# Optimization experiments

Measured on AMD Instinct MI355X. Metric: run time of the kernel, lower is better.

The kernel has to match this reference:

```python
import jax, jax.numpy as jnp
import numpy as np

D_MODEL = 256
N_HEADS = 8
N_LEVELS = 4
N_POINTS = 4
D_FFN = 1024
HW = 128
LQ = HW * HW
LIN = N_LEVELS * LQ
BATCH = 2
HEAD_DIM = D_MODEL // N_HEADS
SPATIAL = [(HW, HW)] * N_LEVELS  # static (H, W) per level
EPS = 1e-5


def _layer_norm(x, g, b):
    m = jnp.mean(x, axis=-1, keepdims=True)
    v = jnp.mean(jnp.square(x - m), axis=-1, keepdims=True)
    return (x - m) * jax.lax.rsqrt(v + EPS) * g + b


def _gather(v, idx):
    # v: (N, heads, HW, hd); idx: (N, heads, Lq, P) -> (N, heads, Lq, P, hd)
    N, Hh, Lq, P = idx.shape
    out = jnp.take_along_axis(v, idx.reshape(N, Hh, Lq * P)[..., None], axis=2)
    return out.reshape(N, Hh, Lq, P, -1)


def _ms_deform_attn_core(value, loc, attn):
    # value: (N, Lin, heads, hd); loc: (N, Lq, heads, L, P, 2) in [0,1]; attn: (N, Lq, heads, L, P)
    N, _, Hh, hd = value.shape
    Lq = loc.shape[1]
    out = jnp.zeros((N, Hh, Lq, hd), value.dtype)
    start = 0
    for l, (H, W) in enumerate(SPATIAL):
        v = value[:, start:start + H * W].transpose(0, 2, 1, 3)  # (N, heads, H*W, hd)
        start += H * W
        ll = loc[:, :, :, l].transpose(0, 2, 1, 3, 4)  # (N, heads, Lq, P, 2)
        # F.grid_sample(align_corners=False, padding_mode='zeros') on grid 2*loc-1:
        # pixel coord = loc * size - 0.5
        x = ll[..., 0] * W - 0.5
        y = ll[..., 1] * H - 0.5
        x0 = jnp.floor(x)
        y0 = jnp.floor(y)
        wx = x - x0
        wy = y - y0
        x0i = x0.astype(jnp.int32)
        y0i = y0.astype(jnp.int32)
        acc = jnp.zeros((N, Hh, Lq, N_POINTS, hd), value.dtype)
        for dy, wyc in ((0, 1.0 - wy), (1, wy)):
            for dx, wxc in ((0, 1.0 - wx), (1, wx)):
                xi = x0i + dx
                yi = y0i + dy
                valid = (xi >= 0) & (xi < W) & (yi >= 0) & (yi < H)
                idx = jnp.clip(yi, 0, H - 1) * W + jnp.clip(xi, 0, W - 1)
                g = _gather(v, idx)
                w = (wxc * wyc * valid).astype(value.dtype)
                acc = acc + g * w[..., None]
        aw = attn[:, :, :, l].transpose(0, 2, 1, 3)  # (N, heads, Lq, P)
        out = out + jnp.sum(acc * aw[..., None], axis=3)
    return out.transpose(0, 2, 1, 3).reshape(N, Lq, Hh * hd)


def _forward(cur_src, src_all, pos, reference_points, spatial_shape,
             W_off, b_off, W_attn, b_attn, W_val, b_val, W_out, b_out,
             gamma1, beta1, W1, b1, W2, b2, gamma2, beta2):
    N, Lq, d = cur_src.shape
    q = cur_src + pos[:, -1]                      # with_pos_embed(cur_src, pos[-1])
    inp = src_all + pos.reshape(N, -1, d)         # with_pos_embed(src_all, cat(pos, 1))
    value = (inp @ W_val + b_val).reshape(N, -1, N_HEADS, HEAD_DIM)
    off = (q @ W_off + b_off).reshape(N, Lq, N_HEADS, N_LEVELS, N_POINTS, 2)
    attn = (q @ W_attn + b_attn).reshape(N, Lq, N_HEADS, N_LEVELS * N_POINTS)
    attn = jax.nn.softmax(attn, axis=-1).reshape(N, Lq, N_HEADS, N_LEVELS, N_POINTS)
    # offset_normalizer = stack([W, H], -1)
    normalizer = jnp.stack([spatial_shape[..., 1], spatial_shape[..., 0]], -1).astype(cur_src.dtype)
    loc = reference_points[:, :, None, :, None, :] + off / normalizer[None, None, None, :, None, :]
    src2 = _ms_deform_attn_core(value, loc, attn) @ W_out + b_out
    src = _layer_norm(cur_src + src2, gamma1, beta1)   # dropout is identity in eval
    ffn = jax.nn.relu(src @ W1 + b1) @ W2 + b2
    return _layer_norm(src + ffn, gamma2, beta2)


def setup_inputs():
    key = jax.random.key(0)
    ks = jax.random.split(key, 16)
    s = 0.02
    f32 = jnp.float32
    return {
        "cur_src": jax.random.normal(ks[0], (BATCH, LQ, D_MODEL), f32),
        "src_all": jax.random.normal(ks[1], (BATCH, LIN, D_MODEL), f32),
        "pos": jax.random.normal(ks[2], (BATCH, N_LEVELS, LQ, D_MODEL), f32),
        "reference_points": jax.random.uniform(ks[3], (BATCH, LQ, N_LEVELS, 2), f32),
        "spatial_shape": jnp.array(SPATIAL, dtype=jnp.int32),
        "level_start_index": (jnp.arange(N_LEVELS) * LQ).astype(jnp.int32),
        "W_off": jax.random.normal(ks[4], (D_MODEL, N_HEADS * N_LEVELS * N_POINTS * 2), f32) * s,
        "b_off": jax.random.normal(ks[5], (N_HEADS * N_LEVELS * N_POINTS * 2,), f32) * 0.5,
        "W_attn": jax.random.normal(ks[6], (D_MODEL, N_HEADS * N_LEVELS * N_POINTS), f32) * s,
        "b_attn": jnp.zeros((N_HEADS * N_LEVELS * N_POINTS,), f32),
        "W_val": jax.random.normal(ks[7], (D_MODEL, D_MODEL), f32) * s,
        "b_val": jnp.zeros((D_MODEL,), f32),
        "W_out": jax.random.normal(ks[8], (D_MODEL, D_MODEL), f32) * s,
        "b_out": jnp.zeros((D_MODEL,), f32),
        "gamma1": jnp.ones((D_MODEL,), f32),
        "beta1": jnp.zeros((D_MODEL,), f32),
        "W1": jax.random.normal(ks[9], (D_MODEL, D_FFN), f32) * s,
        "b1": jnp.zeros((D_FFN,), f32),
        "W2": jax.random.normal(ks[10], (D_FFN, D_MODEL), f32) * s,
        "b2": jnp.zeros((D_MODEL,), f32),
        "gamma2": jnp.ones((D_MODEL,), f32),
        "beta2": jnp.zeros((D_MODEL,), f32),
    }


def reference(cur_src, src_all, pos, reference_points, spatial_shape, level_start_index,
              W_off, b_off, W_attn, b_attn, W_val, b_val, W_out, b_out,
              gamma1, beta1, W1, b1, W2, b2, gamma2, beta2):
    return _forward(cur_src, src_all, pos, reference_points, spatial_shape,
                    W_off, b_off, W_attn, b_attn, W_val, b_val, W_out, b_out,
                    gamma1, beta1, W1, b1, W2, b2, gamma2, beta2)
```

## Files before the change

kernel.cpp:

```cpp
#include <hip/hip_runtime.h>

#define LQN   16384
#define LINN  65536

typedef __attribute__((ext_vector_type(8))) short bf16x8;
typedef __attribute__((ext_vector_type(4))) float f32x4;
typedef __attribute__((ext_vector_type(4))) unsigned short bf16x4;

__device__ __forceinline__ unsigned short f2bf(float f) {
  unsigned u = __float_as_uint(f);
  u += 0x7FFFu + ((u >> 16) & 1u);
  return (unsigned short)(u >> 16);
}

__global__ __launch_bounds__(256) void wtrans6_kernel(
    const float* __restrict__ Wv, const float* __restrict__ Wo,
    const float* __restrict__ Wa, const float* __restrict__ Wu,
    const float* __restrict__ W1, const float* __restrict__ W2,
    unsigned short* __restrict__ wt) {
  int idx = blockIdx.x * 256 + threadIdx.x;
  const float* W; int K, N, base;
  if (idx < 131072) {
    if (idx < 65536) { W = Wv; K = 256; N = 256; base = 0; }
    else             { W = Wo; K = 256; N = 256; base = 65536; }
  } else if (idx < 229376) {
    if (idx < 163840) { W = Wa; K = 256; N = 128; base = 131072; }
    else              { W = Wu; K = 256; N = 256; base = 163840; }
  } else if (idx < 491520) { W = W1; K = 256; N = 1024; base = 229376; }
  else                     { W = W2; K = 1024; N = 256; base = 491520; }
  int local = idx - base;
  int n = local / K, k = local - n * K;
  wt[idx] = f2bf(W[(size_t)k * N + n]);
}

__global__ __launch_bounds__(256) void addcvt_kernel(
    const float* __restrict__ src_all, const float* __restrict__ pos,
    const float* __restrict__ cur, unsigned short* __restrict__ inp_bf,
    unsigned short* __restrict__ qb) {
  size_t i = (size_t)blockIdx.x * 256 + threadIdx.x;
  float4 a = ((const float4*)src_all)[i];
  float4 b = ((const float4*)pos)[i];
  bf16x4 o;
  o.x = f2bf(a.x + b.x); o.y = f2bf(a.y + b.y);
  o.z = f2bf(a.z + b.z); o.w = f2bf(a.w + b.w);
  ((bf16x4*)inp_bf)[i] = o;
  size_t m = i & 4194303;
  if (m >= 3145728) {
    size_t jq = (i >> 22) * 1048576 + (m - 3145728);
    float4 cc = ((const float4*)cur)[jq];
    bf16x4 o2;
    o2.x = f2bf(cc.x + b.x); o2.y = f2bf(cc.y + b.y);
    o2.z = f2bf(cc.z + b.z); o2.w = f2bf(cc.w + b.w);
    ((bf16x4*)qb)[jq] = o2;
  }
}

template <int DO_RELU, int OUT_BF16, int SPLIT>
__global__ __launch_bounds__(256) void gemm_lds_kernel(
    const unsigned short* __restrict__ A, const unsigned short* __restrict__ Bt,
    const float* __restrict__ bias, const float* __restrict__ bias2,
    void* __restrict__ Cp, float* __restrict__ Cp2,
    int M, int N, int K, int ny) {
  __shared__ unsigned short As[128 * 64];
  __shared__ unsigned short Bs[128 * 64];
  const int bid = blockIdx.x;
  const int by = bid % ny, bx = bid / ny;
  const int m0 = bx * 128, n0 = by * 128;
  const int tid = threadIdx.x;
  const int wave = tid >> 6, lane = tid & 63;
  const int wm = (wave >> 1) * 64, wn = (wave & 1) * 64;
  const int l15 = lane & 15, quad = lane >> 4;
  const int rl = lane >> 3;
  const int cl = (lane & 7) ^ rl;

  f32x4 acc[4][4];
#pragma unroll
  for (int i = 0; i < 4; i++)
#pragma unroll
    for (int j = 0; j < 4; j++)
#pragma unroll
      for (int r = 0; r < 4; r++) acc[i][j][r] = 0.f;

  const unsigned short* Abase = A + (size_t)m0 * K + cl * 8;
  const unsigned short* Bbase = Bt + (size_t)n0 * K + cl * 8;

  for (int k0 = 0; k0 < K; k0 += 64) {
#pragma unroll
    for (int t = 0; t < 4; t++) {
      const int row = wave * 32 + t * 8 + rl;
      __builtin_amdgcn_global_load_lds(
          (const __attribute__((address_space(1))) void*)(Abase + (size_t)row * K + k0),
          (__attribute__((address_space(3))) void*)(As + (wave * 32 + t * 8) * 64),
          16, 0, 0);
      __builtin_amdgcn_global_load_lds(
          (const __attribute__((address_space(1))) void*)(Bbase + (size_t)row * K + k0),
          (__attribute__((address_space(3))) void*)(Bs + (wave * 32 + t * 8) * 64),
          16, 0, 0);
    }
    __syncthreads();
#pragma unroll
    for (int kk = 0; kk < 2; kk++) {
      bf16x8 af[4], bfr[4];
#pragma unroll
      for (int i = 0; i < 4; i++) {
        const int row = wm + i * 16 + l15;
        af[i] = *(const bf16x8*)&As[row * 64 + (((quad + 4 * kk) ^ (row & 7)) * 8)];
      }
#pragma unroll
      for (int j = 0; j < 4; j++) {
        const int row = wn + j * 16 + l15;
        bfr[j] = *(const bf16x8*)&Bs[row * 64 + (((quad + 4 * kk) ^ (row & 7)) * 8)];
      }
#pragma unroll
      for (int i = 0; i < 4; i++)
#pragma unroll
        for (int j = 0; j < 4; j++)
          acc[i][j] = __builtin_amdgcn_mfma_f32_16x16x32_bf16(af[i], bfr[j], acc[i][j], 0, 0, 0);
    }
    __syncthreads();
  }
#pragma unroll
  for (int i = 0; i < 4; i++) {
#pragma unroll
    for (int j = 0; j < 4; j++) {
      const int col = n0 + wn + j * 16 + l15;
      float bv;
      if (SPLIT) bv = (col < 256) ? bias[col] : bias2[col - 256];
      else       bv = bias[col];
#pragma unroll
      for (int r = 0; r < 4; r++) {
        const int row = m0 + wm + i * 16 + quad * 4 + r;
        float v = acc[i][j][r] + bv;
        if (DO_RELU) v = fmaxf(v, 0.f);
        if (SPLIT) {
          if (col < 256) ((float*)Cp)[(size_t)row * 256 + col] = v;
          else           Cp2[(size_t)row * 128 + (col - 256)] = v;
        } else if (OUT_BF16) {
          ((unsigned short*)Cp)[(size_t)row * N + col] = f2bf(v);
        } else {
          ((float*)Cp)[(size_t)row * N + col] = v;
        }
      }
    }
  }
}

__global__ __launch_bounds__(256) void sample_kernel(
    const unsigned short* __restrict__ value, const float* __restrict__ offs,
    const float* __restrict__ attnl, const float* __restrict__ refp,
    unsigned int* __restrict__ attn_out) {
  __shared__ float wlds[32 * 16 * 8];
  const int tid = threadIdx.x;
  const int sub = tid >> 3;
  const int cl  = tid & 7;
  const int g = blockIdx.x * 32 + sub;
  const int n = g >> 17;
  const int nl = g >> 3;
  const int h = g & 7;

  const float* lg = attnl + (size_t)nl * 128 + h * 16;
  const float2 l2 = *(const float2*)(lg + 2 * cl);
  float mx = fmaxf(l2.x, l2.y);
#pragma unroll
  for (int o = 1; o < 8; o <<= 1) mx = fmaxf(mx, __shfl_xor(mx, o, 8));
  const float e0 = __expf(l2.x - mx), e1 = __expf(l2.y - mx);
  float s = e0 + e1;
#pragma unroll
  for (int o = 1; o < 8; o <<= 1) s += __shfl_xor(s, o, 8);
  const float inv = 1.f / s;

  const float4 o4 = *(const float4*)(offs + (size_t)g * 32 + 4 * cl);
  const float2 r2 = *(const float2*)(refp + ((size_t)nl * 4 + (cl >> 1)) * 2);
#pragma unroll
  for (int q = 0; q < 2; q++) {
    const float ox = (q == 0) ? o4.x : o4.z;
    const float oy = (q == 0) ? o4.y : o4.w;
    const float aw = ((q == 0) ? e0 : e1) * inv;
    const float x = fmaf(r2.x, 128.f, ox - 0.5f);
    const float y = fmaf(r2.y, 128.f, oy - 0.5f);
    const float xf = floorf(x), yf = floorf(y);
    const float fx = x - xf, fy = y - yf;
    const int x0 = (int)xf, y0 = (int)yf;
    const int xc0 = min(max(x0, 0), 127), xc1 = min(max(x0 + 1, 0), 127);
    const int yc0 = min(max(y0, 0), 127), yc1 = min(max(y0 + 1, 0), 127);
    const float wx0 = (x0 >= 0 && x0 <= 127) ? (1.f - fx) : 0.f;
    const float wx1 = (x0 >= -1 && x0 <= 126) ? fx : 0.f;
    const float wy0 = ((y0 >= 0 && y0 <= 127) ? (1.f - fy) : 0.f) * aw;
    const float wy1 = ((y0 >= -1 && y0 <= 126) ? fy : 0.f) * aw;
    const int p00 = yc0 * 128 + xc0;
    const int p11 = yc1 * 128 + xc1;
    const int dxp = xc1 - xc0;
    const unsigned pk = (unsigned)p00 | ((unsigned)p11 << 14) | ((unsigned)dxp << 28);
    const int pt = 2 * cl + q;
    float4 w4;
    w4.x = wx0 * wy0; w4.y = wx1 * wy0; w4.z = wx0 * wy1; w4.w = wx1 * wy1;
    *(float4*)&wlds[(sub * 16 + pt) * 8] = w4;
    wlds[(sub * 16 + pt) * 8 + 4] = __uint_as_float(pk);
  }

  const char* vb = (const char*)value;
  const unsigned baseidx = ((unsigned)n << 23) + (unsigned)(h * 16 + 2 * cl);
  float a0 = 0.f, a1 = 0.f, a2 = 0.f, a3 = 0.f;
#pragma unroll
  for (int p = 0; p < 16; p++) {
    const float4 w4 = *(const float4*)&wlds[(sub * 16 + p) * 8];
    const unsigned pk = __float_as_uint(wlds[(sub * 16 + p) * 8 + 4]);
    const unsigned lb = (unsigned)(p >> 2) * 2097152u;
    const unsigned p00 = pk & 16383u;
    const unsigned p11 = (pk >> 14) & 16383u;
    const unsigned d128 = (pk >> 28) << 7;
    const unsigned iA = baseidx + (lb + p00 * 128u);
    const unsigned iB = baseidx + (lb + p11 * 128u);
    const uint2 v00 = *(const uint2*)(vb + ((iA) << 2));
    const uint2 v01 = *(const uint2*)(vb + ((iA + d128) << 2));
    const uint2 v11 = *(const uint2*)(vb + ((iB) << 2));
    const uint2 v10 = *(const uint2*)(vb + ((iB - d128) << 2));
#define ACC4(vv, w)                                             \
    a0 = fmaf(w, __uint_as_float((vv).x << 16), a0);            \
    a1 = fmaf(w, __uint_as_float((vv).x & 0xFFFF0000u), a1);    \
    a2 = fmaf(w, __uint_as_float((vv).y << 16), a2);            \
    a3 = fmaf(w, __uint_as_float((vv).y & 0xFFFF0000u), a3);
    ACC4(v00, w4.x)
    ACC4(v01, w4.y)
    ACC4(v10, w4.z)
    ACC4(v11, w4.w)
#undef ACC4
  }
  uint2 o;
  o.x = (unsigned)f2bf(a0) | ((unsigned)f2bf(a1) << 16);
  o.y = (unsigned)f2bf(a2) | ((unsigned)f2bf(a3) << 16);
  ((uint2*)attn_out)[(size_t)g * 8 + cl] = o;
}

template <int EMIT_BF16>
__global__ __launch_bounds__(256) void ln_kernel(const float* __restrict__ x1,
                                                 const float* __restrict__ x2,
                                                 const float* __restrict__ gamma,
                                                 const float* __restrict__ beta,
                                                 float* __restrict__ out,
                                                 unsigned short* __restrict__ outb) {
  const int row = blockIdx.x * 4 + (threadIdx.x >> 6);
  const int lane = threadIdx.x & 63;
  float4 a = ((const float4*)(x1 + (size_t)row * 256))[lane];
  float4 b = ((const float4*)(x2 + (size_t)row * 256))[lane];
  float v0 = a.x + b.x, v1 = a.y + b.y, v2 = a.z + b.z, v3 = a.w + b.w;
  float s1 = v0 + v1 + v2 + v3;
  float s2 = v0 * v0 + v1 * v1 + v2 * v2 + v3 * v3;
#pragma unroll
  for (int o = 1; o < 64; o <<= 1) { s1 += __shfl_xor(s1, o); s2 += __shfl_xor(s2, o); }
  const float mean = s1 * (1.f / 256.f);
  const float var = s2 * (1.f / 256.f) - mean * mean;
  const float rstd = rsqrtf(var + 1e-5f);
  float4 gm = ((const float4*)gamma)[lane];
  float4 bt = ((const float4*)beta)[lane];
  float4 o4;
  o4.x = (v0 - mean) * rstd * gm.x + bt.x;
  o4.y = (v1 - mean) * rstd * gm.y + bt.y;
  o4.z = (v2 - mean) * rstd * gm.z + bt.z;
  o4.w = (v3 - mean) * rstd * gm.w + bt.w;
  ((float4*)(out + (size_t)row * 256))[lane] = o4;
  if (EMIT_BF16) {
    bf16x4 ob;
    ob.x = f2bf(o4.x); ob.y = f2bf(o4.y); ob.z = f2bf(o4.z); ob.w = f2bf(o4.w);
    ((bf16x4*)(outb + (size_t)row * 256))[lane] = ob;
  }
}

extern "C" void kernel_launch(void* const* d_in, const int* in_sizes, int n_in,
                              void* d_out, int out_size, void* d_ws, size_t ws_size,
                              hipStream_t stream) {
  (void)in_sizes; (void)n_in; (void)out_size; (void)ws_size;
  const float* cur_src = (const float*)d_in[0];
  const float* src_all = (const float*)d_in[1];
  const float* pos     = (const float*)d_in[2];
  const float* refp    = (const float*)d_in[3];
  const float* W_off   = (const float*)d_in[6];
  const float* b_off   = (const float*)d_in[7];
  const float* W_attn  = (const float*)d_in[8];
  const float* b_attn  = (const float*)d_in[9];
  const float* W_val   = (const float*)d_in[10];
  const float* b_val   = (const float*)d_in[11];
  const float* W_out   = (const float*)d_in[12];
  const float* b_out   = (const float*)d_in[13];
  const float* gamma1  = (const float*)d_in[14];
  const float* beta1   = (const float*)d_in[15];
  const float* W1      = (const float*)d_in[16];
  const float* b1      = (const float*)d_in[17];
  const float* W2      = (const float*)d_in[18];
  const float* b2      = (const float*)d_in[19];
  const float* gamma2  = (const float*)d_in[20];
  const float* beta2   = (const float*)d_in[21];
  float* out = (float*)d_out;

  char* ws = (char*)d_ws;
  unsigned short* value = (unsigned short*)(ws + 0);
  unsigned short* qbuf  = (unsigned short*)(ws + 67108864);
  float* offbuf         = (float*)(ws + 83886080);
  float* attnl          = (float*)(ws + 117440512);
  unsigned short* attno = (unsigned short*)(ws + 134217728);
  float* src2           = (float*)(ws + 150994944);
  float* srcb           = (float*)(ws + 184549376);
  unsigned short* wt    = (unsigned short*)(ws + 218103808);
  unsigned short* wt_val  = wt;
  unsigned short* wt_qa   = wt + 65536;
  unsigned short* wt_out  = wt + 163840;
  unsigned short* wt_1    = wt + 229376;
  unsigned short* wt_2    = wt + 491520;
  unsigned short* srcb_bf = (unsigned short*)attnl;
  unsigned short* inp_bf  = (unsigned short*)src2;

  wtrans6_kernel<<<2944, 256, 0, stream>>>(W_val, W_off, W_attn, W_out, W1, W2, wt);

  addcvt_kernel<<<32768, 256, 0, stream>>>(src_all, pos, cur_src, inp_bf, qbuf);

  gemm_lds_kernel<0, 1, 0><<<2048, 256, 0, stream>>>(
      inp_bf, wt_val, b_val, nullptr, value, nullptr, 131072, 256, 256, 2);
  gemm_lds_kernel<0, 0, 1><<<768, 256, 0, stream>>>(
      qbuf, wt_qa, b_off, b_attn, offbuf, attnl, 32768, 384, 256, 3);
  sample_kernel<<<8192, 256, 0, stream>>>(value, offbuf, attnl, refp,
                                          (unsigned int*)attno);
  gemm_lds_kernel<0, 0, 0><<<512, 256, 0, stream>>>(
      attno, wt_out, b_out, nullptr, src2, nullptr, 32768, 256, 256, 2);
  ln_kernel<1><<<8192, 256, 0, stream>>>(cur_src, src2, gamma1, beta1, srcb, srcb_bf);
  gemm_lds_kernel<1, 1, 0><<<2048, 256, 0, stream>>>(
      srcb_bf, wt_1, b1, nullptr, value, nullptr, 32768, 1024, 256, 8);
  gemm_lds_kernel<0, 0, 0><<<512, 256, 0, stream>>>(
      value, wt_2, b2, nullptr, offbuf, nullptr, 32768, 256, 1024, 2);
  ln_kernel<0><<<8192, 256, 0, stream>>>(srcb, offbuf, gamma2, beta2, out, nullptr);
}
```

Measured before the change: 652.9 us.

## Store value in head-major layout and sample horizontal pixel pairs per load

The value projection GEMM now writes bf16 output in a per-batch, per-head layout (head, pixel, 32 channels), so the two horizontally adjacent pixels of a bilinear tap are contiguous 128 bytes. The sampler loads 16 bytes per lane covering both left and right pixels, so each point needs two loads (top and bottom rows) instead of four. Left and right halves are then combined with a shuffle. Blocks are reordered head-major so that blocks running together touch the same head slice. The cost is more complex x-clamping and weight-selection logic, scattered stores from the GEMM epilogue, and a shuffle reduction in which half of the lanes idle during the final store.

```diff
diff --git a/kernel.cpp b/kernel.cpp
--- a/kernel.cpp
+++ b/kernel.cpp
@@ -55,7 +55,7 @@
   }
 }
 
-template <int DO_RELU, int OUT_BF16, int SPLIT>
+template <int DO_RELU, int OUT_BF16, int SPLIT, int OUT_VAL>
 __global__ __launch_bounds__(256) void gemm_lds_kernel(
     const unsigned short* __restrict__ A, const unsigned short* __restrict__ Bt,
     const float* __restrict__ bias, const float* __restrict__ bias2,
@@ -136,7 +136,13 @@
           if (col < 256) ((float*)Cp)[(size_t)row * 256 + col] = v;
           else           Cp2[(size_t)row * 128 + (col - 256)] = v;
         } else if (OUT_BF16) {
-          ((unsigned short*)Cp)[(size_t)row * N + col] = f2bf(v);
+          size_t addr;
+          if (OUT_VAL)
+            addr = (((size_t)(row >> 16) * 8 + (col >> 5)) * 65536 +
+                    (size_t)(row & 65535)) * 32 + (col & 31);
+          else
+            addr = (size_t)row * N + col;
+          ((unsigned short*)Cp)[addr] = f2bf(v);
         } else {
           ((float*)Cp)[(size_t)row * N + col] = v;
         }
@@ -149,14 +155,15 @@
     const unsigned short* __restrict__ value, const float* __restrict__ offs,
     const float* __restrict__ attnl, const float* __restrict__ refp,
     unsigned int* __restrict__ attn_out) {
-  __shared__ float wlds[32 * 16 * 8];
+  __shared__ float wlds[32][132];
   const int tid = threadIdx.x;
   const int sub = tid >> 3;
   const int cl  = tid & 7;
-  const int g = blockIdx.x * 32 + sub;
-  const int n = g >> 17;
-  const int nl = g >> 3;
-  const int h = g & 7;
+  const int gb = blockIdx.x * 32 + sub;
+  const int h  = gb >> 15;
+  const int nl = gb & 32767;
+  const int n  = nl >> 14;
+  const int g  = nl * 8 + h;
 
   const float* lg = attnl + (size_t)nl * 128 + h * 16;
   const float2 l2 = *(const float2*)(lg + 2 * cl);
@@ -181,55 +188,59 @@
     const float xf = floorf(x), yf = floorf(y);
     const float fx = x - xf, fy = y - yf;
     const int x0 = (int)xf, y0 = (int)yf;
-    const int xc0 = min(max(x0, 0), 127), xc1 = min(max(x0 + 1, 0), 127);
-    const int yc0 = min(max(y0, 0), 127), yc1 = min(max(y0 + 1, 0), 127);
     const float wx0 = (x0 >= 0 && x0 <= 127) ? (1.f - fx) : 0.f;
     const float wx1 = (x0 >= -1 && x0 <= 126) ? fx : 0.f;
     const float wy0 = ((y0 >= 0 && y0 <= 127) ? (1.f - fy) : 0.f) * aw;
     const float wy1 = ((y0 >= -1 && y0 <= 126) ? fy : 0.f) * aw;
-    const int p00 = yc0 * 128 + xc0;
-    const int p11 = yc1 * 128 + xc1;
-    const int dxp = xc1 - xc0;
-    const unsigned pk = (unsigned)p00 | ((unsigned)p11 << 14) | ((unsigned)dxp << 28);
-    const int pt = 2 * cl + q;
-    float4 w4;
-    w4.x = wx0 * wy0; w4.y = wx1 * wy0; w4.z = wx0 * wy1; w4.w = wx1 * wy1;
-    *(float4*)&wlds[(sub * 16 + pt) * 8] = w4;
-    wlds[(sub * 16 + pt) * 8 + 4] = __uint_as_float(pk);
-  }
-
-  const char* vb = (const char*)value;
-  const unsigned baseidx = ((unsigned)n << 23) + (unsigned)(h * 16 + 2 * cl);
+    const int px = min(max(x0, 0), 126);
+    const float wl = (px == x0) ? wx0 : ((px == x0 + 1) ? wx1 : 0.f);
+    const float wr = (px + 1 == x0) ? wx0 : ((px == x0) ? wx1 : 0.f);
+    const int yc0 = min(max(y0, 0), 127), yc1 = min(max(y0 + 1, 0), 127);
+    const int lb = (cl >> 1) * 16384;
+    const unsigned ot = (unsigned)(lb + yc0 * 128 + px) * 64u;
+    const unsigned ob = (unsigned)(lb + yc1 * 128 + px) * 64u;
+    float* wp = &wlds[sub][(2 * cl + q) * 8];
+    wp[0] = wl * wy0; wp[1] = wr * wy0;
+    wp[2] = wl * wy1; wp[3] = wr * wy1;
+    wp[4] = __uint_as_float(ot); wp[5] = __uint_as_float(ob);
+  }
+
+  const char* hb = (const char*)value + (((size_t)(n * 8 + h)) << 22) + cl * 16;
   float a0 = 0.f, a1 = 0.f, a2 = 0.f, a3 = 0.f;
+  float a4 = 0.f, a5 = 0.f, a6 = 0.f, a7 = 0.f;
 #pragma unroll
   for (int p = 0; p < 16; p++) {
-    const float4 w4 = *(const float4*)&wlds[(sub * 16 + p) * 8];
-    const unsigned pk = __float_as_uint(wlds[(sub * 16 + p) * 8 + 4]);
-    const unsigned lb = (unsigned)(p >> 2) * 2097152u;
-    const unsigned p00 = pk & 16383u;
-    const unsigned p11 = (pk >> 14) & 16383u;
-    const unsigned d128 = (pk >> 28) << 7;
-    const unsigned iA = baseidx + (lb + p00 * 128u);
-    const unsigned iB = baseidx + (lb + p11 * 128u);
-    const uint2 v00 = *(const uint2*)(vb + ((iA) << 2));
-    const uint2 v01 = *(const uint2*)(vb + ((iA + d128) << 2));
-    const uint2 v11 = *(const uint2*)(vb + ((iB) << 2));
-    const uint2 v10 = *(const uint2*)(vb + ((iB - d128) << 2));
-#define ACC4(vv, w)                                             \
-    a0 = fmaf(w, __uint_as_float((vv).x << 16), a0);            \
-    a1 = fmaf(w, __uint_as_float((vv).x & 0xFFFF0000u), a1);    \
-    a2 = fmaf(w, __uint_as_float((vv).y << 16), a2);            \
-    a3 = fmaf(w, __uint_as_float((vv).y & 0xFFFF0000u), a3);
-    ACC4(v00, w4.x)
-    ACC4(v01, w4.y)
-    ACC4(v10, w4.z)
-    ACC4(v11, w4.w)
-#undef ACC4
-  }
-  uint2 o;
-  o.x = (unsigned)f2bf(a0) | ((unsigned)f2bf(a1) << 16);
-  o.y = (unsigned)f2bf(a2) | ((unsigned)f2bf(a3) << 16);
-  ((uint2*)attn_out)[(size_t)g * 8 + cl] = o;
+    const float4 w4 = *(const float4*)&wlds[sub][p * 8];
+    const float2 of2 = *(const float2*)&wlds[sub][p * 8 + 4];
+    const uint4 vt = *(const uint4*)(hb + __float_as_uint(of2.x));
+    const uint4 vb = *(const uint4*)(hb + __float_as_uint(of2.y));
+    const float wtop = (cl < 4) ? w4.x : w4.y;
+    const float wbot = (cl < 4) ? w4.z : w4.w;
+#define ACC8(vv, wgt)                                              \
+    a0 = fmaf(wgt, __uint_as_float((vv).x << 16), a0);             \
+    a1 = fmaf(wgt, __uint_as_float((vv).x & 0xFFFF0000u), a1);     \
+    a2 = fmaf(wgt, __uint_as_float((vv).y << 16), a2);             \
+    a3 = fmaf(wgt, __uint_as_float((vv).y & 0xFFFF0000u), a3);     \
+    a4 = fmaf(wgt, __uint_as_float((vv).z << 16), a4);             \
+    a5 = fmaf(wgt, __uint_as_float((vv).z & 0xFFFF0000u), a5);     \
+    a6 = fmaf(wgt, __uint_as_float((vv).w << 16), a6);             \
+    a7 = fmaf(wgt, __uint_as_float((vv).w & 0xFFFF0000u), a7);
+    ACC8(vt, wtop)
+    ACC8(vb, wbot)
+#undef ACC8
+  }
+  a0 += __shfl_xor(a0, 4, 8); a1 += __shfl_xor(a1, 4, 8);
+  a2 += __shfl_xor(a2, 4, 8); a3 += __shfl_xor(a3, 4, 8);
+  a4 += __shfl_xor(a4, 4, 8); a5 += __shfl_xor(a5, 4, 8);
+  a6 += __shfl_xor(a6, 4, 8); a7 += __shfl_xor(a7, 4, 8);
+  if (cl < 4) {
+    uint4 o;
+    o.x = (unsigned)f2bf(a0) | ((unsigned)f2bf(a1) << 16);
+    o.y = (unsigned)f2bf(a2) | ((unsigned)f2bf(a3) << 16);
+    o.z = (unsigned)f2bf(a4) | ((unsigned)f2bf(a5) << 16);
+    o.w = (unsigned)f2bf(a6) | ((unsigned)f2bf(a7) << 16);
+    ((uint4*)attn_out)[(size_t)g * 4 + cl] = o;
+  }
 }
 
 template <int EMIT_BF16>
@@ -313,18 +324,18 @@
 
   addcvt_kernel<<<32768, 256, 0, stream>>>(src_all, pos, cur_src, inp_bf, qbuf);
 
-  gemm_lds_kernel<0, 1, 0><<<2048, 256, 0, stream>>>(
+  gemm_lds_kernel<0, 1, 0, 1><<<2048, 256, 0, stream>>>(
       inp_bf, wt_val, b_val, nullptr, value, nullptr, 131072, 256, 256, 2);
-  gemm_lds_kernel<0, 0, 1><<<768, 256, 0, stream>>>(
+  gemm_lds_kernel<0, 0, 1, 0><<<768, 256, 0, stream>>>(
       qbuf, wt_qa, b_off, b_attn, offbuf, attnl, 32768, 384, 256, 3);
   sample_kernel<<<8192, 256, 0, stream>>>(value, offbuf, attnl, refp,
                                           (unsigned int*)attno);
-  gemm_lds_kernel<0, 0, 0><<<512, 256, 0, stream>>>(
+  gemm_lds_kernel<0, 0, 0, 0><<<512, 256, 0, stream>>>(
       attno, wt_out, b_out, nullptr, src2, nullptr, 32768, 256, 256, 2);
   ln_kernel<1><<<8192, 256, 0, stream>>>(cur_src, src2, gamma1, beta1, srcb, srcb_bf);
-  gemm_lds_kernel<1, 1, 0><<<2048, 256, 0, stream>>>(
+  gemm_lds_kernel<1, 1, 0, 0><<<2048, 256, 0, stream>>>(
       srcb_bf, wt_1, b1, nullptr, value, nullptr, 32768, 1024, 256, 8);
-  gemm_lds_kernel<0, 0, 0><<<512, 256, 0, stream>>>(
+  gemm_lds_kernel<0, 0, 0, 0><<<512, 256, 0, stream>>>(
       value, wt_2, b2, nullptr, offbuf, nullptr, 32768, 256, 1024, 2);
   ln_kernel<0><<<8192, 256, 0, stream>>>(srcb, offbuf, gamma2, beta2, out, nullptr);
 }
```

Measured after the change: 610.4 us. -6.5%, faster.
